# Kernel optimization log

Measured on AMD Instinct MI355X. Metric: run time of the kernel, lower is better.

The kernel has to match this reference:

```python
import jax, jax.numpy as jnp
import numpy as np

D_FEATURE = 1024
HEAD = 16
D_K = 64
D_V = 64
EPS = 1e-6


def setup_inputs() -> dict:
    key = jax.random.key(0)
    ks = jax.random.split(key, 12)
    B, S = 2, 2048
    s_in = 1.0 / np.sqrt(D_FEATURE)
    s_o = 1.0 / np.sqrt(HEAD * D_V)
    return {
        "q": jax.random.normal(ks[0], (B, S, D_FEATURE), jnp.float32),
        "k": jax.random.normal(ks[1], (B, S, D_FEATURE), jnp.float32),
        "v": jax.random.normal(ks[2], (B, S, D_FEATURE), jnp.float32),
        "Wq": jax.random.uniform(ks[3], (D_FEATURE, HEAD * D_K), jnp.float32, -s_in, s_in),
        "bq": jnp.zeros((HEAD * D_K,), jnp.float32),
        "Wk": jax.random.uniform(ks[4], (D_FEATURE, HEAD * D_K), jnp.float32, -s_in, s_in),
        "bk": jnp.zeros((HEAD * D_K,), jnp.float32),
        "Wv": jax.random.uniform(ks[5], (D_FEATURE, HEAD * D_V), jnp.float32, -s_in, s_in),
        "bv": jnp.zeros((HEAD * D_V,), jnp.float32),
        "Wo": jax.random.uniform(ks[6], (HEAD * D_V, D_FEATURE), jnp.float32, -s_o, s_o),
        "bo": jnp.zeros((D_FEATURE,), jnp.float32),
        "gamma": jnp.ones((D_FEATURE,), jnp.float32),
        "beta": jnp.zeros((D_FEATURE,), jnp.float32),
    }


def reference(q, k, v, Wq, bq, Wk, bk, Wv, bv, Wo, bo, gamma, beta):
    B, Sq, _ = q.shape
    Sk, Sv = k.shape[1], v.shape[1]
    shortcut = v
    # projections -> (b, h, s, d)
    qh = (q @ Wq + bq).reshape(B, Sq, HEAD, D_K).transpose(0, 2, 1, 3)
    kh = (k @ Wk + bk).reshape(B, Sk, HEAD, D_K).transpose(0, 2, 1, 3)
    vh = (v @ Wv + bv).reshape(B, Sv, HEAD, D_V).transpose(0, 2, 1, 3)
    scale = 1.0 / np.sqrt(D_K).astype(np.float32)
    scores = jnp.einsum('bhqd,bhkd->bhqk', qh * scale, kh)
    attn = jax.nn.softmax(scores, axis=-1)  # dropout is identity (p=0 / eval)
    ctx = jnp.einsum('bhqk,bhkd->bhqd', attn, vh)
    ctx = ctx.transpose(0, 2, 1, 3).reshape(B, Sv, HEAD * D_V)
    out = ctx @ Wo + bo
    out = out + shortcut
    # LayerNorm, eps=1e-6
    mu = out.mean(-1, keepdims=True)
    var = out.var(-1, keepdims=True)
    out = (out - mu) * jax.lax.rsqrt(var + EPS) * gamma + beta
    return out
```

## Files before the change

### kernel.cpp

```cpp
#include <hip/hip_runtime.h>

#define D_FEAT 1024
#define NTOK   4096
#define SEQ    2048
#define NHEAD  16
#define DK     64
#define QSCALE 0.1803368801111204f

typedef float          f32x4  __attribute__((ext_vector_type(4)));
typedef float          f32x16 __attribute__((ext_vector_type(16)));
typedef short          s16x8  __attribute__((ext_vector_type(8)));
typedef unsigned short u16x4  __attribute__((ext_vector_type(4)));

__device__ __forceinline__ unsigned short f2bf(float f) {
  union { float f; unsigned int u; } x; x.f = f;
  unsigned int r = x.u + 0x7fffu + ((x.u >> 16) & 1u);
  return (unsigned short)(r >> 16);
}
__device__ __forceinline__ unsigned short f2h(float f) {
  union { _Float16 h; unsigned short u; } x; x.h = (_Float16)f; return x.u;
}
__device__ __forceinline__ float h2f(unsigned short u) {
  union { _Float16 h; unsigned short u; } x; x.u = u; return (float)x.h;
}

__device__ __forceinline__ f32x4 mfma16(s16x8 a, s16x8 b, f32x4 c) {
  return __builtin_amdgcn_mfma_f32_16x16x32_bf16(a, b, c, 0, 0, 0);
}
__device__ __forceinline__ f32x16 mfma32(s16x8 a, s16x8 b, f32x16 c) {
  return __builtin_amdgcn_mfma_f32_32x32x16_bf16(a, b, c, 0, 0, 0);
}

__device__ __forceinline__ void gload16(const void* g, void* l) {
  __builtin_amdgcn_global_load_lds(
      (const __attribute__((address_space(1))) void*)g,
      (__attribute__((address_space(3))) void*)l, 16, 0, 0);
}

__device__ __forceinline__ float fexp2(float x) {
  return __builtin_amdgcn_exp2f(x);
}

__device__ __forceinline__ unsigned int cvtpk(float a, float b) {
  unsigned int r;
  asm("v_cvt_pk_bf16_f32 %0, %1, %2" : "=v"(r) : "v"(a), "v"(b));
  return r;
}
__device__ __forceinline__ void swap32(unsigned int& x, unsigned int& y) {
  asm("v_permlane32_swap_b32 %0, %1" : "+v"(x), "+v"(y));
}
__device__ __forceinline__ s16x8 mk8(unsigned int a, unsigned int b,
                                     unsigned int c, unsigned int d) {
  union { unsigned int u[4]; s16x8 v; } x;
  x.u[0] = a; x.u[1] = b; x.u[2] = c; x.u[3] = d; return x.v;
}

__global__ __launch_bounds__(256) void prep_kernel(
    const float* __restrict__ q, const float* __restrict__ k, const float* __restrict__ v,
    const float* __restrict__ Wq, const float* __restrict__ Wk,
    const float* __restrict__ Wv, const float* __restrict__ Wo,
    unsigned short* __restrict__ qb, unsigned short* __restrict__ kb,
    unsigned short* __restrict__ vb,
    unsigned short* __restrict__ WT, unsigned short* __restrict__ Wot)
{
  __shared__ float tile[32][33];
  const int bx = blockIdx.x, tid = threadIdx.x;
  if (bx < 12288) {
    int sel = bx >> 12;
    const float* src = sel == 0 ? q : (sel == 1 ? k : v);
    unsigned short* dst = sel == 0 ? qb : (sel == 1 ? kb : vb);
    size_t i = ((size_t)(bx & 4095) * 256 + tid) * 4;
    float4 f = *(const float4*)(src + i);
    u16x4 o; o.x = f2bf(f.x); o.y = f2bf(f.y); o.z = f2bf(f.z); o.w = f2bf(f.w);
    *(u16x4*)(dst + i) = o;
  } else {
    int t = bx - 12288;
    int z = t >> 10, rest = t & 1023;
    int bxt = rest & 31, byt = rest >> 5;
    const float* W = z == 0 ? Wq : z == 1 ? Wk : z == 2 ? Wv : Wo;
    unsigned short* T = (z < 3) ? (WT + (size_t)z * 1024 * 1024) : Wot;
    int tx = tid & 31, ty = tid >> 5;
    int n = bxt * 32 + tx;
    for (int i = 0; i < 4; ++i) {
      int kk = byt * 32 + ty + i * 8;
      tile[ty + i * 8][tx] = W[(size_t)kk * D_FEAT + n];
    }
    __syncthreads();
    int kk = byt * 32 + tx;
    for (int i = 0; i < 4; ++i) {
      int n2 = bxt * 32 + ty + i * 8;
      T[(size_t)n2 * D_FEAT + kk] = f2bf(tile[tx][ty + i * 8]);
    }
  }
}

__global__ __launch_bounds__(256, 3) void gemm_qkv(
    const unsigned short* __restrict__ qb, const unsigned short* __restrict__ kb,
    const unsigned short* __restrict__ vb, const unsigned short* __restrict__ WT,
    const float* __restrict__ bq, const float* __restrict__ bk, const float* __restrict__ bv,
    unsigned short* __restrict__ Qp, unsigned short* __restrict__ Kp, unsigned short* __restrict__ Vt)
{
  __shared__ __align__(16) unsigned short sAB[2 * 128 * 64];
  unsigned short* sA = sAB;
  unsigned short* sB = sAB + 128 * 64;
  const int tid = threadIdx.x;
  const int wave = tid >> 6, lane = tid & 63;
  const int quad = lane >> 4, l16 = lane & 15;
  const int wx = wave & 1, wy = wave >> 1;
  const int bx = blockIdx.x;
  const int chunk = bx >> 3;

  const unsigned short* rA;
  const unsigned short* rB;
  int m0, n0;
  if (chunk < 2) {
    m0 = blockIdx.y * 128; n0 = (bx & 7) * 128;
    rA = (chunk ? kb : qb) + (size_t)m0 * D_FEAT;
    rB = WT + (size_t)(chunk * 1024 + n0) * D_FEAT;
  } else {
    m0 = (bx & 7) * 128; n0 = blockIdx.y * 128;
    rA = WT + (size_t)(2048 + m0) * D_FEAT;
    rB = vb + (size_t)n0 * D_FEAT;
  }

  f32x4 acc[4][4];
  for (int mt = 0; mt < 4; ++mt)
    for (int nt = 0; nt < 4; ++nt) acc[mt][nt] = (f32x4){0.f, 0.f, 0.f, 0.f};

  const int rw8 = lane >> 3;
  const int cls = ((lane & 7) ^ (lane >> 3)) * 8;
  const int sw = l16 & 7;

  for (int k0 = 0; k0 < D_FEAT; k0 += 64) {
    __syncthreads();
    for (int j = 0; j < 4; ++j) {
      int ch = wave * 4 + j;
      gload16(rA + (size_t)(ch * 8 + rw8) * D_FEAT + k0 + cls, sA + ch * 512);
      gload16(rB + (size_t)(ch * 8 + rw8) * D_FEAT + k0 + cls, sB + ch * 512);
    }
    __syncthreads();
    s16x8 af[2][4], bfr[2][4];
    for (int kk = 0; kk < 2; ++kk) {
      int c = ((kk * 4 + quad) ^ sw) * 8;
      for (int mt = 0; mt < 4; ++mt)
        af[kk][mt] = *(const s16x8*)(sA + (wy * 64 + mt * 16 + l16) * 64 + c);
      for (int nt = 0; nt < 4; ++nt)
        bfr[kk][nt] = *(const s16x8*)(sB + (wx * 64 + nt * 16 + l16) * 64 + c);
    }
    for (int kk = 0; kk < 2; ++kk)
      for (int mt = 0; mt < 4; ++mt)
        for (int nt = 0; nt < 4; ++nt)
          acc[mt][nt] = mfma16(af[kk][mt], bfr[kk][nt], acc[mt][nt]);
  }

  if (chunk < 2) {
    const float* bias = chunk ? bk : bq;
    unsigned short* Cp = chunk ? Kp : Qp;
    const float scale = chunk == 0 ? QSCALE : 1.0f;
    for (int mt = 0; mt < 4; ++mt)
      for (int nt = 0; nt < 4; ++nt) {
        int col = n0 + wx * 64 + nt * 16 + l16;
        float bcol = bias[col];
        for (int r = 0; r < 4; ++r) {
          int row = m0 + wy * 64 + mt * 16 + quad * 4 + r;
          Cp[(size_t)row * D_FEAT + col] = f2bf((acc[mt][nt][r] + bcol) * scale);
        }
      }
  } else {
    for (int mt = 0; mt < 4; ++mt)
      for (int r = 0; r < 4; ++r) {
        float bfeat = bv[m0 + wy * 64 + mt * 16 + quad * 4 + r];
        for (int nt = 0; nt < 4; ++nt) acc[mt][nt][r] += bfeat;
      }
    unsigned short* tb = sAB;
    for (int p = 0; p < 2; ++p) {
      __syncthreads();
      if (wx == p) {
        for (int mt = 0; mt < 4; ++mt)
          for (int nt = 0; nt < 4; ++nt) {
            int tok_loc = nt * 16 + l16;
            for (int r = 0; r < 4; ++r) {
              int f_loc = wy * 64 + mt * 16 + quad * 4 + r;
              tb[f_loc * 72 + tok_loc] = f2bf(acc[mt][nt][r]);
            }
          }
      }
      __syncthreads();
      int n_base = n0 + p * 64;
      int b = n_base >> 11, tok0 = n_base & 2047;
      int ck = lane & 7;
      for (int j = 0; j < 4; ++j) {
        int f_loc = (wave * 4 + j) * 8 + rw8;
        int f = m0 + f_loc, hh = f >> 6, dv = f & 63;
        *(s16x8*)(Vt + ((size_t)(b * 16 + hh) * 64 + dv) * SEQ + tok0 + ck * 8) =
            *(const s16x8*)(tb + f_loc * 72 + ck * 8);
      }
    }
  }
}

__global__ __launch_bounds__(256) void gemm_o(
    const unsigned short* __restrict__ A, const unsigned short* __restrict__ Bt,
    const float* __restrict__ bias, const float* __restrict__ resid,
    float* __restrict__ Cout)
{
  __shared__ __align__(16) unsigned short sA[128 * 64];
  __shared__ __align__(16) unsigned short sB[64 * 64];
  const int tid = threadIdx.x;
  const int wave = tid >> 6, lane = tid & 63;
  const int quad = lane >> 4, l16 = lane & 15;
  const int wx = wave & 1, wy = wave >> 1;
  const int n0 = blockIdx.x * 64, m0 = blockIdx.y * 128;

  f32x4 acc[4][2];
  for (int mt = 0; mt < 4; ++mt)
    for (int nt = 0; nt < 2; ++nt) acc[mt][nt] = (f32x4){0.f, 0.f, 0.f, 0.f};

  const int rw8 = lane >> 3;
  const int cls = ((lane & 7) ^ (lane >> 3)) * 8;
  const int sw = l16 & 7;

  for (int k0 = 0; k0 < D_FEAT; k0 += 64) {
    __syncthreads();
    for (int j = 0; j < 4; ++j) {
      int ch = wave * 4 + j;
      gload16(A + (size_t)(m0 + ch * 8 + rw8) * D_FEAT + k0 + cls, sA + ch * 512);
    }
    for (int j = 0; j < 2; ++j) {
      int ch = wave * 2 + j;
      gload16(Bt + (size_t)(n0 + ch * 8 + rw8) * D_FEAT + k0 + cls, sB + ch * 512);
    }
    __syncthreads();
    s16x8 af[2][4], bfr[2][2];
    for (int kk = 0; kk < 2; ++kk) {
      int c = ((kk * 4 + quad) ^ sw) * 8;
      for (int mt = 0; mt < 4; ++mt)
        af[kk][mt] = *(const s16x8*)(sA + (wy * 64 + mt * 16 + l16) * 64 + c);
      for (int nt = 0; nt < 2; ++nt)
        bfr[kk][nt] = *(const s16x8*)(sB + (wx * 32 + nt * 16 + l16) * 64 + c);
    }
    for (int kk = 0; kk < 2; ++kk)
      for (int mt = 0; mt < 4; ++mt)
        for (int nt = 0; nt < 2; ++nt)
          acc[mt][nt] = mfma16(af[kk][mt], bfr[kk][nt], acc[mt][nt]);
  }

  for (int mt = 0; mt < 4; ++mt)
    for (int nt = 0; nt < 2; ++nt) {
      int col = n0 + wx * 32 + nt * 16 + l16;
      float bcol = bias[col];
      for (int r = 0; r < 4; ++r) {
        int row = m0 + wy * 64 + mt * 16 + quad * 4 + r;
        Cout[(size_t)row * D_FEAT + col] =
            acc[mt][nt][r] + bcol + resid[(size_t)row * D_FEAT + col];
      }
    }
}

__global__ __launch_bounds__(256, 4) void flash_part(
    const unsigned short* __restrict__ Qp,
    const unsigned short* __restrict__ Kp,
    const unsigned short* __restrict__ Vt,
    unsigned short* __restrict__ Opart,
    float* __restrict__ L)
{
  __shared__ __align__(16) unsigned short sB3[3][4096];

  const int tid = threadIdx.x;
  const int wave = tid >> 6, lane = tid & 63;
  const int l32 = lane & 31, h = lane >> 5;

  const int blk = blockIdx.x;
  const int xcd = blk & 7, jj = blk >> 3;
  const int grp = xcd * 8 + (jj >> 4);
  const int q0 = (jj & 15) * 128;
  const int bh = grp & 31, z = grp >> 5;
  const int b = bh >> 4, hd = bh & 15;
  const int kbase = z * (SEQ / 2);
  const size_t base = (size_t)b * SEQ * D_FEAT + (size_t)hd * DK;
  const unsigned short* vt = Vt + (size_t)bh * 64 * SEQ;

  const int qrow = wave * 32 + l32;

  const unsigned short* qptr = Qp + base + (size_t)(q0 + qrow) * D_FEAT;
  s16x8 bq[4];
#pragma unroll
  for (int s = 0; s < 4; ++s)
    bq[s] = *(const s16x8*)(qptr + (2 * s + h) * 8);

  const int krow = tid >> 3;
  const unsigned short* kPtr =
      Kp + base + (size_t)(kbase + krow) * D_FEAT + (((tid & 7) ^ (krow & 7)) * 8);
  const int vrow = tid >> 2;
  const unsigned short* vPtr =
      vt + (size_t)vrow * SEQ + kbase + (((tid & 3) ^ (vrow & 3)) * 8);

  const int kdst = wave * 512;
  gload16(kPtr, &sB3[0][kdst]);
  gload16(vPtr, &sB3[0][2048 + kdst]);
  kPtr += 32 * D_FEAT; vPtr += 32;
  gload16(kPtr, &sB3[1][kdst]);
  gload16(vPtr, &sB3[1][2048 + kdst]);
  kPtr += 32 * D_FEAT; vPtr += 32;

  f32x16 o0, o1;
#pragma unroll
  for (int r = 0; r < 16; ++r) { o0[r] = 0.f; o1[r] = 0.f; }
  float lsA = 0.f, lsB = 0.f;

  const int kxor = l32 & 7;
  const int vxor = l32 & 3;
  const int NT = (SEQ / 2) / 32;

#define FLASH_TILE(BUF)                                                        \
  {                                                                            \
    const unsigned short* bK = &sB3[BUF][0];                                   \
    const unsigned short* bV = &sB3[BUF][2048];                                \
    f32x16 st;                                                                 \
    _Pragma("unroll") for (int r = 0; r < 16; ++r) st[r] = 0.f;                \
    __builtin_amdgcn_s_setprio(1);                                            \
    _Pragma("unroll") for (int s = 0; s < 4; ++s) {                            \
      s16x8 a = *(const s16x8*)(bK + l32 * 64 + (((2 * s + h) ^ kxor) * 8));   \
      st = mfma32(a, bq[s], st);                                               \
    }                                                                          \
    __builtin_amdgcn_s_setprio(0);                                            \
    unsigned int c[8];                                                         \
    _Pragma("unroll") for (int i = 0; i < 8; ++i) {                            \
      float e0 = fexp2(st[2 * i]);                                             \
      float e1 = fexp2(st[2 * i + 1]);                                         \
      lsA += e0; lsB += e1;                                                    \
      c[i] = cvtpk(e0, e1);                                                    \
    }                                                                          \
    swap32(c[0], c[2]); swap32(c[1], c[3]);                                    \
    swap32(c[4], c[6]); swap32(c[5], c[7]);                                    \
    s16x8 bp0 = mk8(c[0], c[1], c[2], c[3]);                  \
    s16x8 bp1 = mk8(c[4], c[5], c[6], c[7]);                  \
    __builtin_amdgcn_s_setprio(1);                                            \
    _Pragma("unroll") for (int kk = 0; kk < 2; ++kk) {                         \
      int cs = ((2 * kk + h) ^ vxor) * 8;                                      \
      s16x8 av0 = *(const s16x8*)(bV + l32 * 32 + cs);                         \
      s16x8 av1 = *(const s16x8*)(bV + (32 + l32) * 32 + cs);                  \
      s16x8 bp = kk ? bp1 : bp0;                                               \
      o0 = mfma32(av0, bp, o0);                                                \
      o1 = mfma32(av1, bp, o1);                                                \
    }                                                                          \
    __builtin_amdgcn_s_setprio(0);                                            \
  }

#define FLASH_STEP(CURB, NXT2B)                                                \
  {                                                                            \
    asm volatile("s_waitcnt vmcnt(2)" ::: "memory");                           \
    __builtin_amdgcn_s_barrier();                                             \
    __builtin_amdgcn_sched_barrier(0);                                        \
    gload16(kPtr, &sB3[NXT2B][kdst]);                                          \
    gload16(vPtr, &sB3[NXT2B][2048 + kdst]);                                   \
    kPtr += 32 * D_FEAT; vPtr += 32;                                           \
    FLASH_TILE(CURB);                                                          \
  }

  for (int t3 = 0; t3 < NT - 2; t3 += 3) {
    FLASH_STEP(0, 2);
    FLASH_STEP(1, 0);
    FLASH_STEP(2, 1);
  }
  asm volatile("s_waitcnt vmcnt(2)" ::: "memory");
  __builtin_amdgcn_s_barrier();
  __builtin_amdgcn_sched_barrier(0);
  FLASH_TILE(0);
  asm volatile("s_waitcnt vmcnt(0)" ::: "memory");
  __builtin_amdgcn_s_barrier();
  __builtin_amdgcn_sched_barrier(0);
  FLASH_TILE(1);
#undef FLASH_STEP
#undef FLASH_TILE

  float lsum = lsA + lsB;
  lsum += __shfl_xor(lsum, 32, 64);
  const size_t trow = (size_t)(z * 32 + bh) * SEQ + (q0 + qrow);
  unsigned short* orow = Opart + trow * 64;
#pragma unroll
  for (int g = 0; g < 4; ++g) {
    u16x4 ov;
    for (int r = 0; r < 4; ++r) ov[r] = f2h(o0[4 * g + r]);
    *(u16x4*)(orow + 8 * g + 4 * h) = ov;
  }
#pragma unroll
  for (int g = 0; g < 4; ++g) {
    u16x4 ov;
    for (int r = 0; r < 4; ++r) ov[r] = f2h(o1[4 * g + r]);
    *(u16x4*)(orow + 32 + 8 * g + 4 * h) = ov;
  }
  if (h == 0) L[trow] = lsum;
}

__global__ __launch_bounds__(256) void combine_kernel(
    const unsigned short* __restrict__ Opart, const float* __restrict__ L,
    unsigned short* __restrict__ ctx)
{
  const int idx = blockIdx.x * 256 + threadIdx.x;
  const int dq = idx & 15;
  const int trow = idx >> 4;
  const int bh = trow >> 11, tok = trow & 2047;
  const int b = bh >> 4, h = bh & 15;
  const int HS = 32 * SEQ;

  float inv = __builtin_amdgcn_rcpf(L[trow] + L[HS + trow]);

  u16x4 p0 = *(const u16x4*)(Opart + (size_t)trow * 64 + dq * 4);
  u16x4 p1 = *(const u16x4*)(Opart + ((size_t)HS + trow) * 64 + dq * 4);
  u16x4 o;
  for (int r = 0; r < 4; ++r)
    o[r] = f2bf((h2f(p0[r]) + h2f(p1[r])) * inv);
  *(u16x4*)(ctx + (size_t)b * SEQ * D_FEAT + (size_t)tok * D_FEAT + h * 64 + dq * 4) = o;
}

__global__ __launch_bounds__(256) void ln_kernel(
    const float* __restrict__ x, const float* __restrict__ gamma,
    const float* __restrict__ beta, float* __restrict__ out)
{
  const int row = blockIdx.x, tid = threadIdx.x;
  const int wave = tid >> 6, lane = tid & 63;
  const float* xr = x + (size_t)row * D_FEAT;
  float4 v = ((const float4*)xr)[tid];
  float s  = v.x + v.y + v.z + v.w;
  float ss = v.x * v.x + v.y * v.y + v.z * v.z + v.w * v.w;
  for (int off = 1; off < 64; off <<= 1) {
    s  += __shfl_xor(s,  off, 64);
    ss += __shfl_xor(ss, off, 64);
  }
  __shared__ float red[8];
  if (lane == 0) { red[wave] = s; red[wave + 4] = ss; }
  __syncthreads();
  s  = red[0] + red[1] + red[2] + red[3];
  ss = red[4] + red[5] + red[6] + red[7];
  float mean = s * (1.f / D_FEAT);
  float var  = ss * (1.f / D_FEAT) - mean * mean;
  float rstd = rsqrtf(var + 1e-6f);
  float4 g  = ((const float4*)gamma)[tid];
  float4 bt = ((const float4*)beta)[tid];
  float4 o;
  o.x = (v.x - mean) * rstd * g.x + bt.x;
  o.y = (v.y - mean) * rstd * g.y + bt.y;
  o.z = (v.z - mean) * rstd * g.z + bt.z;
  o.w = (v.w - mean) * rstd * g.w + bt.w;
  ((float4*)(out + (size_t)row * D_FEAT))[tid] = o;
}

extern "C" void kernel_launch(void* const* d_in, const int* in_sizes, int n_in,
                              void* d_out, int out_size, void* d_ws, size_t ws_size,
                              hipStream_t stream) {
  const float* q     = (const float*)d_in[0];
  const float* k     = (const float*)d_in[1];
  const float* v     = (const float*)d_in[2];
  const float* Wq    = (const float*)d_in[3];
  const float* bq    = (const float*)d_in[4];
  const float* Wk    = (const float*)d_in[5];
  const float* bk    = (const float*)d_in[6];
  const float* Wv    = (const float*)d_in[7];
  const float* bv    = (const float*)d_in[8];
  const float* Wo    = (const float*)d_in[9];
  const float* bo    = (const float*)d_in[10];
  const float* gamma = (const float*)d_in[11];
  const float* beta  = (const float*)d_in[12];

  char* w = (char*)d_ws;
  const size_t MB = 1u << 20;
  unsigned short* qb    = (unsigned short*)(w + 0 * MB);
  unsigned short* kb    = (unsigned short*)(w + 8 * MB);
  unsigned short* vb    = (unsigned short*)(w + 16 * MB);
  unsigned short* WT    = (unsigned short*)(w + 24 * MB);
  unsigned short* Wot   = (unsigned short*)(w + 30 * MB);
  unsigned short* Qp    = (unsigned short*)(w + 32 * MB);
  unsigned short* Kp    = (unsigned short*)(w + 40 * MB);
  unsigned short* Vt    = (unsigned short*)(w + 48 * MB);
  unsigned short* ctx   = (unsigned short*)(w + 56 * MB);
  float*          tmp   = (float*)(w + 64 * MB);
  unsigned short* Opart = (unsigned short*)(w + 0 * MB);
  float*          L     = (float*)(w + 16 * MB);

  prep_kernel<<<16384, 256, 0, stream>>>(q, k, v, Wq, Wk, Wv, Wo, qb, kb, vb, WT, Wot);

  gemm_qkv<<<dim3(24, 32), 256, 0, stream>>>(qb, kb, vb, WT, bq, bk, bv, Qp, Kp, Vt);

  flash_part<<<1024, 256, 0, stream>>>(Qp, Kp, Vt, Opart, L);

  combine_kernel<<<4096, 256, 0, stream>>>(Opart, L, ctx);

  gemm_o<<<dim3(16, 32), 256, 0, stream>>>(ctx, Wot, bo, v, tmp);

  ln_kernel<<<NTOK, 256, 0, stream>>>(tmp, gamma, beta, (float*)d_out);
}
```

Baseline: 232.9 us.

## Process two query tiles per flash block to reuse K/V shared-memory tiles

Each flash_part block now handles 256 query rows (two 128-row sets A and B) instead of 128, so every K/V tile staged in LDS feeds twice as many MFMAs. The grid is halved, occupancy hint dropped from 4 to 2 blocks per CU, and the V swizzle pattern is changed. This cuts global/LDS load traffic per unit of compute but doubles accumulator registers and lowers parallelism, with only 512 blocks left.

```diff
diff --git a/kernel.cpp b/kernel.cpp
--- a/kernel.cpp
+++ b/kernel.cpp
@@ -257,7 +257,7 @@
     }
 }
 
-__global__ __launch_bounds__(256, 4) void flash_part(
+__global__ __launch_bounds__(256, 2) void flash_part(
     const unsigned short* __restrict__ Qp,
     const unsigned short* __restrict__ Kp,
     const unsigned short* __restrict__ Vt,
@@ -272,8 +272,8 @@
 
   const int blk = blockIdx.x;
   const int xcd = blk & 7, jj = blk >> 3;
-  const int grp = xcd * 8 + (jj >> 4);
-  const int q0 = (jj & 15) * 128;
+  const int grp = xcd * 8 + (jj >> 3);
+  const int q0 = (jj & 7) * 256;
   const int bh = grp & 31, z = grp >> 5;
   const int b = bh >> 4, hd = bh & 15;
   const int kbase = z * (SEQ / 2);
@@ -282,18 +282,21 @@
 
   const int qrow = wave * 32 + l32;
 
-  const unsigned short* qptr = Qp + base + (size_t)(q0 + qrow) * D_FEAT;
-  s16x8 bq[4];
+  const unsigned short* qptrA = Qp + base + (size_t)(q0 + qrow) * D_FEAT;
+  const unsigned short* qptrB = qptrA + (size_t)128 * D_FEAT;
+  s16x8 bqA[4], bqB[4];
 #pragma unroll
-  for (int s = 0; s < 4; ++s)
-    bq[s] = *(const s16x8*)(qptr + (2 * s + h) * 8);
+  for (int s = 0; s < 4; ++s) {
+    bqA[s] = *(const s16x8*)(qptrA + (2 * s + h) * 8);
+    bqB[s] = *(const s16x8*)(qptrB + (2 * s + h) * 8);
+  }
 
   const int krow = tid >> 3;
   const unsigned short* kPtr =
       Kp + base + (size_t)(kbase + krow) * D_FEAT + (((tid & 7) ^ (krow & 7)) * 8);
   const int vrow = tid >> 2;
   const unsigned short* vPtr =
-      vt + (size_t)vrow * SEQ + kbase + (((tid & 3) ^ (vrow & 3)) * 8);
+      vt + (size_t)vrow * SEQ + kbase + (((tid & 3) ^ ((tid >> 3) & 3)) * 8);
 
   const int kdst = wave * 512;
   gload16(kPtr, &sB3[0][kdst]);
@@ -303,46 +306,54 @@
   gload16(vPtr, &sB3[1][2048 + kdst]);
   kPtr += 32 * D_FEAT; vPtr += 32;
 
-  f32x16 o0, o1;
+  f32x16 o0A, o1A, o0B, o1B;
 #pragma unroll
-  for (int r = 0; r < 16; ++r) { o0[r] = 0.f; o1[r] = 0.f; }
-  float lsA = 0.f, lsB = 0.f;
+  for (int r = 0; r < 16; ++r) { o0A[r] = 0.f; o1A[r] = 0.f; o0B[r] = 0.f; o1B[r] = 0.f; }
+  float lsA0 = 0.f, lsA1 = 0.f, lsB0 = 0.f, lsB1 = 0.f;
 
   const int kxor = l32 & 7;
-  const int vxor = l32 & 3;
+  const int vxor = (l32 >> 1) & 3;
   const int NT = (SEQ / 2) / 32;
 
 #define FLASH_TILE(BUF)                                                        \
   {                                                                            \
     const unsigned short* bK = &sB3[BUF][0];                                   \
     const unsigned short* bV = &sB3[BUF][2048];                                \
-    f32x16 st;                                                                 \
-    _Pragma("unroll") for (int r = 0; r < 16; ++r) st[r] = 0.f;                \
+    f32x16 stA, stB;                                                           \
+    _Pragma("unroll") for (int r = 0; r < 16; ++r) { stA[r] = 0.f; stB[r] = 0.f; } \
     __builtin_amdgcn_s_setprio(1);                                            \
     _Pragma("unroll") for (int s = 0; s < 4; ++s) {                            \
       s16x8 a = *(const s16x8*)(bK + l32 * 64 + (((2 * s + h) ^ kxor) * 8));   \
-      st = mfma32(a, bq[s], st);                                               \
+      stA = mfma32(a, bqA[s], stA);                                            \
+      stB = mfma32(a, bqB[s], stB);                                            \
     }                                                                          \
     __builtin_amdgcn_s_setprio(0);                                            \
-    unsigned int c[8];                                                         \
+    unsigned int cA[8], cB[8];                                                 \
     _Pragma("unroll") for (int i = 0; i < 8; ++i) {                            \
-      float e0 = fexp2(st[2 * i]);                                             \
-      float e1 = fexp2(st[2 * i + 1]);                                         \
-      lsA += e0; lsB += e1;                                                    \
-      c[i] = cvtpk(e0, e1);                                                    \
+      float a0 = fexp2(stA[2 * i]), a1 = fexp2(stA[2 * i + 1]);                \
+      lsA0 += a0; lsA1 += a1; cA[i] = cvtpk(a0, a1);                           \
+      float b0 = fexp2(stB[2 * i]), b1 = fexp2(stB[2 * i + 1]);                \
+      lsB0 += b0; lsB1 += b1; cB[i] = cvtpk(b0, b1);                           \
     }                                                                          \
-    swap32(c[0], c[2]); swap32(c[1], c[3]);                                    \
-    swap32(c[4], c[6]); swap32(c[5], c[7]);                                    \
-    s16x8 bp0 = mk8(c[0], c[1], c[2], c[3]);                  \
-    s16x8 bp1 = mk8(c[4], c[5], c[6], c[7]);                  \
+    swap32(cA[0], cA[2]); swap32(cA[1], cA[3]);                                \
+    swap32(cA[4], cA[6]); swap32(cA[5], cA[7]);                                \
+    swap32(cB[0], cB[2]); swap32(cB[1], cB[3]);                                \
+    swap32(cB[4], cB[6]); swap32(cB[5], cB[7]);                                \
+    s16x8 bpA0 = mk8(cA[0], cA[1], cA[2], cA[3]);                              \
+    s16x8 bpA1 = mk8(cA[4], cA[5], cA[6], cA[7]);                              \
+    s16x8 bpB0 = mk8(cB[0], cB[1], cB[2], cB[3]);                              \
+    s16x8 bpB1 = mk8(cB[4], cB[5], cB[6], cB[7]);                              \
     __builtin_amdgcn_s_setprio(1);                                            \
     _Pragma("unroll") for (int kk = 0; kk < 2; ++kk) {                         \
       int cs = ((2 * kk + h) ^ vxor) * 8;                                      \
       s16x8 av0 = *(const s16x8*)(bV + l32 * 32 + cs);                         \
       s16x8 av1 = *(const s16x8*)(bV + (32 + l32) * 32 + cs);                  \
-      s16x8 bp = kk ? bp1 : bp0;                                               \
-      o0 = mfma32(av0, bp, o0);                                                \
-      o1 = mfma32(av1, bp, o1);                                                \
+      s16x8 bpA = kk ? bpA1 : bpA0;                                            \
+      s16x8 bpB = kk ? bpB1 : bpB0;                                            \
+      o0A = mfma32(av0, bpA, o0A);                                             \
+      o1A = mfma32(av1, bpA, o1A);                                             \
+      o0B = mfma32(av0, bpB, o0B);                                             \
+      o1B = mfma32(av1, bpB, o1B);                                             \
     }                                                                          \
     __builtin_amdgcn_s_setprio(0);                                            \
   }
@@ -374,23 +385,27 @@
 #undef FLASH_STEP
 #undef FLASH_TILE
 
-  float lsum = lsA + lsB;
-  lsum += __shfl_xor(lsum, 32, 64);
-  const size_t trow = (size_t)(z * 32 + bh) * SEQ + (q0 + qrow);
-  unsigned short* orow = Opart + trow * 64;
+  float lsumA = lsA0 + lsA1;
+  lsumA += __shfl_xor(lsumA, 32, 64);
+  float lsumB = lsB0 + lsB1;
+  lsumB += __shfl_xor(lsumB, 32, 64);
+  const size_t trowA = (size_t)(z * 32 + bh) * SEQ + (q0 + qrow);
+  const size_t trowB = trowA + 128;
+  unsigned short* orowA = Opart + trowA * 64;
+  unsigned short* orowB = Opart + trowB * 64;
 #pragma unroll
   for (int g = 0; g < 4; ++g) {
     u16x4 ov;
-    for (int r = 0; r < 4; ++r) ov[r] = f2h(o0[4 * g + r]);
-    *(u16x4*)(orow + 8 * g + 4 * h) = ov;
-  }
-#pragma unroll
-  for (int g = 0; g < 4; ++g) {
-    u16x4 ov;
-    for (int r = 0; r < 4; ++r) ov[r] = f2h(o1[4 * g + r]);
-    *(u16x4*)(orow + 32 + 8 * g + 4 * h) = ov;
-  }
-  if (h == 0) L[trow] = lsum;
+    for (int r = 0; r < 4; ++r) ov[r] = f2h(o0A[4 * g + r]);
+    *(u16x4*)(orowA + 8 * g + 4 * h) = ov;
+    for (int r = 0; r < 4; ++r) ov[r] = f2h(o1A[4 * g + r]);
+    *(u16x4*)(orowA + 32 + 8 * g + 4 * h) = ov;
+    for (int r = 0; r < 4; ++r) ov[r] = f2h(o0B[4 * g + r]);
+    *(u16x4*)(orowB + 8 * g + 4 * h) = ov;
+    for (int r = 0; r < 4; ++r) ov[r] = f2h(o1B[4 * g + r]);
+    *(u16x4*)(orowB + 32 + 8 * g + 4 * h) = ov;
+  }
+  if (h == 0) { L[trowA] = lsumA; L[trowB] = lsumB; }
 }
 
 __global__ __launch_bounds__(256) void combine_kernel(
@@ -482,7 +497,7 @@
 
   gemm_qkv<<<dim3(24, 32), 256, 0, stream>>>(qb, kb, vb, WT, bq, bk, bv, Qp, Kp, Vt);
 
-  flash_part<<<1024, 256, 0, stream>>>(Qp, Kp, Vt, Opart, L);
+  flash_part<<<512, 256, 0, stream>>>(Qp, Kp, Vt, Opart, L);
 
   combine_kernel<<<4096, 256, 0, stream>>>(Opart, L, ctx);
 
```

New measurement: 230.1 us. No clear change (-1.2%).

## Software-pipeline flash QK and softmax-PV across tiles with four LDS buffers

Applied to the files above, without the earlier changes.

Splits the flash tile into a QK^T MFMA stage and an exp/PV stage, then interleaves the QK of tile i+1 with the softmax and PV of tile i so exp work overlaps matrix work. The LDS ring grows from three to four buffers and occupancy hint drops from 4 to 3 blocks per CU to make room for an extra score accumulator. The V swizzle pattern also changes to a different XOR key. A buffer could be overwritten while still being read if the ordering is off, and lower occupancy may reduce latency hiding.

```diff
diff --git a/kernel.cpp b/kernel.cpp
--- a/kernel.cpp
+++ b/kernel.cpp
@@ -257,14 +257,14 @@
     }
 }
 
-__global__ __launch_bounds__(256, 4) void flash_part(
+__global__ __launch_bounds__(256, 3) void flash_part(
     const unsigned short* __restrict__ Qp,
     const unsigned short* __restrict__ Kp,
     const unsigned short* __restrict__ Vt,
     unsigned short* __restrict__ Opart,
     float* __restrict__ L)
 {
-  __shared__ __align__(16) unsigned short sB3[3][4096];
+  __shared__ __align__(16) unsigned short sB4[4][4096];
 
   const int tid = threadIdx.x;
   const int wave = tid >> 6, lane = tid & 63;
@@ -293,41 +293,43 @@
       Kp + base + (size_t)(kbase + krow) * D_FEAT + (((tid & 7) ^ (krow & 7)) * 8);
   const int vrow = tid >> 2;
   const unsigned short* vPtr =
-      vt + (size_t)vrow * SEQ + kbase + (((tid & 3) ^ (vrow & 3)) * 8);
+      vt + (size_t)vrow * SEQ + kbase + (((tid & 3) ^ ((tid >> 3) & 3)) * 8);
 
   const int kdst = wave * 512;
-  gload16(kPtr, &sB3[0][kdst]);
-  gload16(vPtr, &sB3[0][2048 + kdst]);
-  kPtr += 32 * D_FEAT; vPtr += 32;
-  gload16(kPtr, &sB3[1][kdst]);
-  gload16(vPtr, &sB3[1][2048 + kdst]);
-  kPtr += 32 * D_FEAT; vPtr += 32;
-
-  f32x16 o0, o1;
+#pragma unroll
+  for (int pb = 0; pb < 2; ++pb) {
+    gload16(kPtr, &sB4[pb][kdst]);
+    gload16(vPtr, &sB4[pb][2048 + kdst]);
+    kPtr += 32 * D_FEAT; vPtr += 32;
+  }
+
+  f32x16 o0, o1, stE, stO;
 #pragma unroll
   for (int r = 0; r < 16; ++r) { o0[r] = 0.f; o1[r] = 0.f; }
   float lsA = 0.f, lsB = 0.f;
 
   const int kxor = l32 & 7;
-  const int vxor = l32 & 3;
-  const int NT = (SEQ / 2) / 32;
-
-#define FLASH_TILE(BUF)                                                        \
+  const int vxor = (l32 >> 1) & 3;
+
+#define QK_TILE(BUF, ST)                                                       \
   {                                                                            \
-    const unsigned short* bK = &sB3[BUF][0];                                   \
-    const unsigned short* bV = &sB3[BUF][2048];                                \
-    f32x16 st;                                                                 \
-    _Pragma("unroll") for (int r = 0; r < 16; ++r) st[r] = 0.f;                \
+    const unsigned short* bK = &sB4[BUF][0];                                   \
+    _Pragma("unroll") for (int r = 0; r < 16; ++r) ST[r] = 0.f;                \
     __builtin_amdgcn_s_setprio(1);                                            \
     _Pragma("unroll") for (int s = 0; s < 4; ++s) {                            \
       s16x8 a = *(const s16x8*)(bK + l32 * 64 + (((2 * s + h) ^ kxor) * 8));   \
-      st = mfma32(a, bq[s], st);                                               \
+      ST = mfma32(a, bq[s], ST);                                               \
     }                                                                          \
     __builtin_amdgcn_s_setprio(0);                                            \
+  }
+
+#define SMPV_TILE(BUFV, ST)                                                    \
+  {                                                                            \
+    const unsigned short* bV = &sB4[BUFV][2048];                               \
     unsigned int c[8];                                                         \
     _Pragma("unroll") for (int i = 0; i < 8; ++i) {                            \
-      float e0 = fexp2(st[2 * i]);                                             \
-      float e1 = fexp2(st[2 * i + 1]);                                         \
+      float e0 = fexp2(ST[2 * i]);                                             \
+      float e1 = fexp2(ST[2 * i + 1]);                                         \
       lsA += e0; lsB += e1;                                                    \
       c[i] = cvtpk(e0, e1);                                                    \
     }                                                                          \
@@ -347,32 +349,37 @@
     __builtin_amdgcn_s_setprio(0);                                            \
   }
 
-#define FLASH_STEP(CURB, NXT2B)                                                \
-  {                                                                            \
-    asm volatile("s_waitcnt vmcnt(2)" ::: "memory");                           \
-    __builtin_amdgcn_s_barrier();                                             \
-    __builtin_amdgcn_sched_barrier(0);                                        \
-    gload16(kPtr, &sB3[NXT2B][kdst]);                                          \
-    gload16(vPtr, &sB3[NXT2B][2048 + kdst]);                                   \
-    kPtr += 32 * D_FEAT; vPtr += 32;                                           \
-    FLASH_TILE(CURB);                                                          \
-  }
-
-  for (int t3 = 0; t3 < NT - 2; t3 += 3) {
-    FLASH_STEP(0, 2);
-    FLASH_STEP(1, 0);
-    FLASH_STEP(2, 1);
-  }
-  asm volatile("s_waitcnt vmcnt(2)" ::: "memory");
-  __builtin_amdgcn_s_barrier();
+#define SYNC2                                                                  \
+  asm volatile("s_waitcnt vmcnt(2)" ::: "memory");                             \
+  __builtin_amdgcn_s_barrier();                                               \
   __builtin_amdgcn_sched_barrier(0);
-  FLASH_TILE(0);
+#define ISSUE(NXT)                                                             \
+  gload16(kPtr, &sB4[NXT][kdst]);                                              \
+  gload16(vPtr, &sB4[NXT][2048 + kdst]);                                       \
+  kPtr += 32 * D_FEAT; vPtr += 32;
+
+  SYNC2; ISSUE(2); QK_TILE(0, stE);
+  SYNC2; ISSUE(3); QK_TILE(1, stO); SMPV_TILE(0, stE);
+  SYNC2; ISSUE(0); QK_TILE(2, stE); SMPV_TILE(1, stO);
+  SYNC2; ISSUE(1); QK_TILE(3, stO); SMPV_TILE(2, stE);
+  for (int g6 = 0; g6 < 6; ++g6) {
+    SYNC2; ISSUE(2); QK_TILE(0, stE); SMPV_TILE(3, stO);
+    SYNC2; ISSUE(3); QK_TILE(1, stO); SMPV_TILE(0, stE);
+    SYNC2; ISSUE(0); QK_TILE(2, stE); SMPV_TILE(1, stO);
+    SYNC2; ISSUE(1); QK_TILE(3, stO); SMPV_TILE(2, stE);
+  }
+  SYNC2; ISSUE(2); QK_TILE(0, stE); SMPV_TILE(3, stO);
+  SYNC2; ISSUE(3); QK_TILE(1, stO); SMPV_TILE(0, stE);
+  SYNC2;           QK_TILE(2, stE); SMPV_TILE(1, stO);
   asm volatile("s_waitcnt vmcnt(0)" ::: "memory");
   __builtin_amdgcn_s_barrier();
   __builtin_amdgcn_sched_barrier(0);
-  FLASH_TILE(1);
-#undef FLASH_STEP
-#undef FLASH_TILE
+  QK_TILE(3, stO); SMPV_TILE(2, stE);
+  SMPV_TILE(3, stO);
+#undef QK_TILE
+#undef SMPV_TILE
+#undef SYNC2
+#undef ISSUE
 
   float lsum = lsA + lsB;
   lsum += __shfl_xor(lsum, 32, 64);
```

Result: no change. 230.2 us (-1.2%).
